# Kernel tuning notes

Measured on AMD Instinct MI355X. Metric: run time of the kernel, lower is better.

The kernel has to match this reference:

```python
import jax, jax.numpy as jnp
import numpy as np


def setup_inputs() -> dict:
    key = jax.random.key(0)
    k1, k2 = jax.random.split(key)
    B, C, T = 32, 64, 8192
    y_pred = jax.random.normal(k1, (B, C, T), dtype=jnp.float32)
    y_true = jax.random.normal(k2, (B, C, T), dtype=jnp.float32)
    return {"y_pred": y_pred, "y_true": y_true}


def reference(y_pred, y_true):
    # Faithful to the torch code: the triu mask multiply + sum over the second
    # time axis is exactly abs_diff[b,c,t] weighted by row-sum of triu = (T - t).
    # channel_sums then sums over t and c; final reduction is a mean over batch.
    B, C, T = y_pred.shape
    abs_diff = jnp.abs(y_pred - y_true)                      # (B, C, T)
    w = jnp.arange(T, 0, -1, dtype=abs_diff.dtype)           # weight[t] = T - t
    per_batch = jnp.einsum('bct,t->b', abs_diff, w)          # (B,)
    scaling = 2.0 / (T * C * (T + 1))                        # apply_scaling_factor=True
    return scaling * jnp.mean(per_batch)
```

## Files before the change

### kernel.cpp

```cpp
#include <hip/hip_runtime.h>


#define T_DIM 8192
#define T_MASK 8191

__global__ __launch_bounds__(256)
void WassersteinLoss_kernel(const float4* __restrict__ a,
                            const float4* __restrict__ b,
                            float* __restrict__ out,
                            int n4, float scale) {
    int tid = blockIdx.x * blockDim.x + threadIdx.x;
    int stride = gridDim.x * blockDim.x;

    float acc = 0.0f;
    for (int v = tid; v < n4; v += stride) {
        float4 x = a[v];
        float4 y = b[v];
        int t = (v << 2) & T_MASK;
        float w = (float)(T_DIM - t);
        float d0 = fabsf(x.x - y.x);
        float d1 = fabsf(x.y - y.y);
        float d2 = fabsf(x.z - y.z);
        float d3 = fabsf(x.w - y.w);
        acc += w * (d0 + d1 + d2 + d3) - (d1 + 2.0f * d2 + 3.0f * d3);
    }

    #pragma unroll
    for (int off = 32; off > 0; off >>= 1)
        acc += __shfl_down(acc, off, 64);

    __shared__ float wave_sums[4];
    int lane = threadIdx.x & 63;
    int wave = threadIdx.x >> 6;
    if (lane == 0) wave_sums[wave] = acc;
    __syncthreads();

    if (threadIdx.x == 0) {
        float s = wave_sums[0] + wave_sums[1] + wave_sums[2] + wave_sums[3];
        atomicAdd(out, s * scale);
    }
}

extern "C" void kernel_launch(void* const* d_in, const int* in_sizes, int n_in,
                              void* d_out, int out_size, void* d_ws, size_t ws_size,
                              hipStream_t stream) {
    const float* a = (const float*)d_in[0];
    const float* b = (const float*)d_in[1];
    float* out = (float*)d_out;

    int n = in_sizes[0];
    int n4 = n >> 2;

    const long long T = T_DIM;
    const long long C = 64;
    const long long B = (long long)n / (C * T);
    float scale = (float)(2.0 / ((double)T * (double)C * (double)(T + 1) * (double)B));

    hipMemsetAsync(out, 0, sizeof(float) * out_size, stream);

    const int threads = 256;
    const int blocks = 2048;
    WassersteinLoss_kernel<<<blocks, threads, 0, stream>>>(
        (const float4*)a, (const float4*)b, out, n4, scale);
}
```

Baseline: 159.6 us.

## Batch loads for memory parallelism and replace atomics with two-pass reduction

The grid-stride loop now issues eight float4 loads from each input before doing any arithmetic, so more memory requests are in flight per thread. The final reduction also changes: each block writes its partial sum to workspace and a second single-block kernel sums them and applies the scale, replacing the memset plus atomicAdd. This adds a second kernel launch and raises register pressure in exchange for more memory-level parallelism and a deterministic reduction.

```diff
diff --git a/kernel.cpp b/kernel.cpp
--- a/kernel.cpp
+++ b/kernel.cpp
@@ -3,21 +3,40 @@
 
 #define T_DIM 8192
 #define T_MASK 8191
+#define BATCH 8
 
 __global__ __launch_bounds__(256)
-void WassersteinLoss_kernel(const float4* __restrict__ a,
-                            const float4* __restrict__ b,
-                            float* __restrict__ out,
-                            int n4, float scale) {
+void wl_partial_kernel(const float4* __restrict__ a,
+                       const float4* __restrict__ b,
+                       float* __restrict__ partial,
+                       int n4) {
     int tid = blockIdx.x * blockDim.x + threadIdx.x;
     int stride = gridDim.x * blockDim.x;
 
     float acc = 0.0f;
-    for (int v = tid; v < n4; v += stride) {
+    int v = tid;
+
+    for (; v + (BATCH - 1) * stride < n4; v += BATCH * stride) {
+        float4 xa[BATCH], xb[BATCH];
+        #pragma unroll
+        for (int i = 0; i < BATCH; ++i) xa[i] = a[v + i * stride];
+        #pragma unroll
+        for (int i = 0; i < BATCH; ++i) xb[i] = b[v + i * stride];
+        #pragma unroll
+        for (int i = 0; i < BATCH; ++i) {
+            int idx = v + i * stride;
+            float w = (float)(T_DIM - ((idx << 2) & T_MASK));
+            float d0 = fabsf(xa[i].x - xb[i].x);
+            float d1 = fabsf(xa[i].y - xb[i].y);
+            float d2 = fabsf(xa[i].z - xb[i].z);
+            float d3 = fabsf(xa[i].w - xb[i].w);
+            acc += w * (d0 + d1 + d2 + d3) - (d1 + 2.0f * d2 + 3.0f * d3);
+        }
+    }
+    for (; v < n4; v += stride) {
         float4 x = a[v];
         float4 y = b[v];
-        int t = (v << 2) & T_MASK;
-        float w = (float)(T_DIM - t);
+        float w = (float)(T_DIM - ((v << 2) & T_MASK));
         float d0 = fabsf(x.x - y.x);
         float d1 = fabsf(x.y - y.y);
         float d2 = fabsf(x.z - y.z);
@@ -35,10 +54,29 @@
     if (lane == 0) wave_sums[wave] = acc;
     __syncthreads();
 
-    if (threadIdx.x == 0) {
-        float s = wave_sums[0] + wave_sums[1] + wave_sums[2] + wave_sums[3];
-        atomicAdd(out, s * scale);
-    }
+    if (threadIdx.x == 0)
+        partial[blockIdx.x] = wave_sums[0] + wave_sums[1] + wave_sums[2] + wave_sums[3];
+}
+
+__global__ __launch_bounds__(256)
+void wl_final_kernel(const float* __restrict__ partial, int n,
+                     float* __restrict__ out, float scale) {
+    float acc = 0.0f;
+    for (int i = threadIdx.x; i < n; i += 256)
+        acc += partial[i];
+
+    #pragma unroll
+    for (int off = 32; off > 0; off >>= 1)
+        acc += __shfl_down(acc, off, 64);
+
+    __shared__ float wave_sums[4];
+    int lane = threadIdx.x & 63;
+    int wave = threadIdx.x >> 6;
+    if (lane == 0) wave_sums[wave] = acc;
+    __syncthreads();
+
+    if (threadIdx.x == 0)
+        out[0] = (wave_sums[0] + wave_sums[1] + wave_sums[2] + wave_sums[3]) * scale;
 }
 
 extern "C" void kernel_launch(void* const* d_in, const int* in_sizes, int n_in,
@@ -47,6 +85,7 @@
     const float* a = (const float*)d_in[0];
     const float* b = (const float*)d_in[1];
     float* out = (float*)d_out;
+    float* partial = (float*)d_ws;
 
     int n = in_sizes[0];
     int n4 = n >> 2;
@@ -56,10 +95,9 @@
     const long long B = (long long)n / (C * T);
     float scale = (float)(2.0 / ((double)T * (double)C * (double)(T + 1) * (double)B));
 
-    hipMemsetAsync(out, 0, sizeof(float) * out_size, stream);
-
     const int threads = 256;
     const int blocks = 2048;
-    WassersteinLoss_kernel<<<blocks, threads, 0, stream>>>(
-        (const float4*)a, (const float4*)b, out, n4, scale);
+    wl_partial_kernel<<<blocks, threads, 0, stream>>>(
+        (const float4*)a, (const float4*)b, partial, n4);
+    wl_final_kernel<<<1, threads, 0, stream>>>(partial, blocks, out, scale);
 }
```

New measurement: 146.1 us. -8.5%, faster.
